# Kernel tuning notes

Hardware: AMD Instinct MI355X
Metric: run time of the kernel (lower is better)

The kernel has to match this reference:

```python
import jax, jax.numpy as jnp
import numpy as np

N_NODES = 32
GAT_OUT = 64
LSTM_H = 128
N_CLS = 4
NEG_SLOPE = 0.2


def setup_inputs() -> dict:
    key = jax.random.key(0)
    ks = jax.random.split(key, 12)
    B, T, E = 32, 512, 96
    F, H = GAT_OUT, LSTM_H
    s = 0.05
    return {
        "x_seq": jax.random.normal(ks[0], (B, T, N_NODES), jnp.float32),
        "edge_index": jax.random.randint(ks[1], (2, E), 0, N_NODES, jnp.int32),
        # GATConv params (heads=1): lin weight [in=1, F], attention vectors [F], bias [F]
        "w_gat": jax.random.normal(ks[2], (1, F), jnp.float32) * s,
        "att_src": jax.random.normal(ks[3], (F,), jnp.float32) * s,
        "att_dst": jax.random.normal(ks[4], (F,), jnp.float32) * s,
        "b_gat": jnp.zeros((F,), jnp.float32),
        # LSTM params, torch gate order (i, f, g, o)
        "W_ih": jax.random.normal(ks[5], (N_NODES * F, 4 * H), jnp.float32) * s,
        "W_hh": jax.random.normal(ks[6], (H, 4 * H), jnp.float32) * s,
        "b_ih": jnp.zeros((4 * H,), jnp.float32),
        "b_hh": jnp.zeros((4 * H,), jnp.float32),
        # classifier
        "W_fc": jax.random.normal(ks[7], (H, N_CLS), jnp.float32) * s,
        "b_fc": jnp.zeros((N_CLS,), jnp.float32),
    }


def _forward(x_seq, edge_index, w_gat, att_src, att_dst, b_gat,
             W_ih, W_hh, b_ih, b_hh, W_fc, b_fc):
    B, T, N = x_seq.shape
    F = w_gat.shape[1]
    H = W_hh.shape[0]

    # --- GAT over all (B,T) steps at once (PyG GATConv, heads=1, self-loops) ---
    loops = jnp.arange(N, dtype=edge_index.dtype)
    src = jnp.concatenate([edge_index[0], loops])  # [Et]
    dst = jnp.concatenate([edge_index[1], loops])  # [Et]
    Et = src.shape[0]

    h = x_seq[..., None] * w_gat            # [B,T,N,F] (in_channels=1 linear)
    a_s = h @ att_src                        # [B,T,N]
    a_d = h @ att_dst                        # [B,T,N]
    e = a_s[..., src] + a_d[..., dst]        # [B,T,Et]
    e = jnp.where(e > 0, e, NEG_SLOPE * e)   # LeakyReLU(0.2)

    # segment softmax over destination node, batched over B*T
    e2 = jnp.moveaxis(e, -1, 0).reshape(Et, B * T)
    m = jax.ops.segment_max(e2, dst, num_segments=N)        # [N,B*T]
    ex = jnp.exp(e2 - m[dst])
    z = jax.ops.segment_sum(ex, dst, num_segments=N)        # [N,B*T]
    alpha = ex / z[dst]                                      # [Et,B*T]
    alpha = jnp.moveaxis(alpha.reshape(Et, B, T), 0, -1)     # [B,T,Et]

    msg = alpha[..., None] * h[:, :, src, :]                 # [B,T,Et,F]
    onehot = (dst[:, None] == jnp.arange(N)).astype(h.dtype)  # [Et,N]
    out = jnp.einsum('btef,en->btnf', msg, onehot) + b_gat    # [B,T,N,F]

    seq = out.reshape(B, T, N * F)           # [B,T,2048]

    # --- single-layer LSTM (batch_first), torch gate order i,f,g,o ---
    xw = seq @ W_ih + (b_ih + b_hh)          # [B,T,4H]

    def step(carry, xw_t):
        hs, cs = carry
        g = xw_t + hs @ W_hh                 # [B,4H]
        i, f, gg, o = jnp.split(g, 4, axis=-1)
        cs = jax.nn.sigmoid(f) * cs + jax.nn.sigmoid(i) * jnp.tanh(gg)
        hs = jax.nn.sigmoid(o) * jnp.tanh(cs)
        return (hs, cs), None

    h0 = jnp.zeros((B, H), seq.dtype)
    (h_last, _), _ = jax.lax.scan(step, (h0, h0), jnp.moveaxis(xw, 1, 0))

    return h_last @ W_fc + b_fc              # [B,num_classes]


def reference(x_seq, edge_index, w_gat, att_src, att_dst, b_gat,
              W_ih, W_hh, b_ih, b_hh, W_fc, b_fc):
    return _forward(x_seq, edge_index, w_gat, att_src, att_dst, b_gat,
                    W_ih, W_hh, b_ih, b_hh, W_fc, b_fc)
```

## Files before the change

### kernel.cpp

```cpp
#include <hip/hip_runtime.h>

#define NN 32
#define FF 64
#define HH 128
#define G4 512
#define BB 32
#define TT 512
#define ET 128
#define NPOS (BB*TT)

__device__ __forceinline__ float frcp(float x) { return __builtin_amdgcn_rcpf(x); }

__global__ __launch_bounds__(512) void prep_kernel(const float* __restrict__ w_gat,
                                                   const float* __restrict__ b_gat,
                                                   const float* __restrict__ W_ih,
                                                   float* __restrict__ W_eff,
                                                   float* __restrict__ biasp) {
  int j = threadIdx.x;
  int n = blockIdx.x;
  float accw = 0.f, accb = 0.f;
#pragma unroll 8
  for (int f = 0; f < FF; ++f) {
    float wv = W_ih[(n * FF + f) * G4 + j];
    accw = fmaf(w_gat[f], wv, accw);
    accb = fmaf(b_gat[f], wv, accb);
  }
  W_eff[n * G4 + j] = accw;
  biasp[n * G4 + j] = accb;
}

__global__ __launch_bounds__(512) void prep2_kernel(const float* __restrict__ biasp,
                                                    const float* __restrict__ b_ih,
                                                    const float* __restrict__ b_hh,
                                                    const float* __restrict__ w_gat,
                                                    const float* __restrict__ att_src,
                                                    const float* __restrict__ att_dst,
                                                    const int* __restrict__ ei,
                                                    float* __restrict__ bias_eff,
                                                    float* __restrict__ scal,
                                                    int* __restrict__ srt_g,
                                                    int* __restrict__ off_g) {
  __shared__ int cnt[NN];
  __shared__ int off[NN + 1];
  __shared__ int srt[ET];
  int j = threadIdx.x;
  if (j < NN) cnt[j] = 0;
  float acc = b_ih[j] + b_hh[j];
#pragma unroll
  for (int n = 0; n < NN; ++n) acc += biasp[n * G4 + j];
  bias_eff[j] = acc;
  if (j == 0) {
    float cs = 0.f, cd = 0.f;
    for (int f = 0; f < FF; ++f) {
      cs = fmaf(w_gat[f], att_src[f], cs);
      cd = fmaf(w_gat[f], att_dst[f], cd);
    }
    scal[0] = cs;
    scal[1] = cd;
  }
  __syncthreads();
  int s = 0, d = 0, tk = 0;
  if (j < ET) {
    if (j < 96) { s = ei[j]; d = ei[96 + j]; }
    else { s = j - 96; d = j - 96; }
    tk = atomicAdd(&cnt[d], 1);
  }
  __syncthreads();
  if (j == 0) {
    off[0] = 0;
    for (int n = 0; n < NN; ++n) off[n + 1] = off[n] + cnt[n];
  }
  __syncthreads();
  if (j < ET) srt[off[d] + tk] = s;
  __syncthreads();
  if (j < ET) srt_g[j] = srt[j];
  if (j < NN + 1) off_g[j] = off[j];
}

__global__ __launch_bounds__(128) void prep3_kernel(const float* __restrict__ W_hh,
                                                    float* __restrict__ Wt) {
  int tid = blockIdx.x;
  int m = threadIdx.x;
  int r = tid >> 2, kq = tid & 3;
  int g = m >> 5, kk = m & 31;
  Wt[tid * 128 + m] = W_hh[(kq * 32 + kk) * G4 + g * 128 + r];
}

__global__ __launch_bounds__(256) void gatxw_kernel(const float* __restrict__ x_seq,
                                                    const int* __restrict__ srt_g,
                                                    const int* __restrict__ off_g,
                                                    const float* __restrict__ scal,
                                                    const float* __restrict__ W_eff,
                                                    const float* __restrict__ bias_eff,
                                                    float* __restrict__ xw) {
  __shared__ int srt[ET];
  __shared__ int offs[NN + 1];
  __shared__ float xs[8 * 32];
  __shared__ float sl[8 * 32];
  int tid = threadIdx.x;
  int posbase = blockIdx.x * 8;
  float we0[NN], we1[NN];
#pragma unroll
  for (int nn = 0; nn < NN; ++nn) {
    we0[nn] = W_eff[nn * G4 + tid];
    we1[nn] = W_eff[nn * G4 + 256 + tid];
  }
  float b0 = bias_eff[tid], b1 = bias_eff[256 + tid];
  if (tid < ET) srt[tid] = srt_g[tid];
  if (tid < NN + 1) offs[tid] = off_g[tid];
  int p = tid >> 5, n = tid & 31;
  xs[tid] = x_seq[posbase * NN + tid];
  __syncthreads();
  float cs = scal[0], cd = scal[1];
  int base = p * 32;
  int e0 = offs[n], e1 = offs[n + 1];
  float xn = xs[base + n];
  float cdxn = cd * xn;
  float m = -3.0e38f;
  for (int e = e0; e < e1; ++e) {
    float ev = fmaf(cs, xs[base + srt[e]], cdxn);
    ev = ev > 0.f ? ev : 0.2f * ev;
    m = fmaxf(m, ev);
  }
  float z = 0.f, sa = 0.f;
  for (int e = e0; e < e1; ++e) {
    float xsv = xs[base + srt[e]];
    float ev = fmaf(cs, xsv, cdxn);
    ev = ev > 0.f ? ev : 0.2f * ev;
    float ex = __expf(ev - m);
    z += ex;
    sa = fmaf(ex, xsv, sa);
  }
  sl[p * 32 + n] = sa * frcp(z);
  __syncthreads();
  for (int pp = 0; pp < 8; ++pp) {
    const float4* sp = (const float4*)&sl[pp * 32];
    float a0 = b0, a1 = b1;
#pragma unroll
    for (int q = 0; q < 8; ++q) {
      float4 sv = sp[q];
      a0 = fmaf(sv.x, we0[4 * q], a0);
      a0 = fmaf(sv.y, we0[4 * q + 1], a0);
      a0 = fmaf(sv.z, we0[4 * q + 2], a0);
      a0 = fmaf(sv.w, we0[4 * q + 3], a0);
      a1 = fmaf(sv.x, we1[4 * q], a1);
      a1 = fmaf(sv.y, we1[4 * q + 1], a1);
      a1 = fmaf(sv.z, we1[4 * q + 2], a1);
      a1 = fmaf(sv.w, we1[4 * q + 3], a1);
    }
    size_t row = (size_t)(posbase + pp) * G4;
    xw[row + tid] = a0;
    xw[row + 256 + tid] = a1;
  }
}


#define PK16F(HP, W0, W1, W2, W3) \
  "v_pk_fma_f32 v[216:217], v[" HP "], v[" W0 "], 0\n\t" \
  "v_pk_fma_f32 v[218:219], v[" HP "], v[" W1 "], 0\n\t" \
  "v_pk_fma_f32 v[220:221], v[" HP "], v[" W2 "], 0\n\t" \
  "v_pk_fma_f32 v[222:223], v[" HP "], v[" W3 "], 0\n\t"

#define PK16A(HP, W0, W1, W2, W3) \
  "v_pk_fma_f32 v[216:217], v[" HP "], v[" W0 "], v[216:217]\n\t" \
  "v_pk_fma_f32 v[218:219], v[" HP "], v[" W1 "], v[218:219]\n\t" \
  "v_pk_fma_f32 v[220:221], v[" HP "], v[" W2 "], v[220:221]\n\t" \
  "v_pk_fma_f32 v[222:223], v[" HP "], v[" W3 "], v[222:223]\n\t"

#define PHASE(XSLOT, RD, WR) \
  "ds_read_b128 v[32:35], " RD "\n\t" \
  "ds_read_b128 v[36:39], " RD " offset:16\n\t" \
  "ds_read_b128 v[40:43], " RD " offset:32\n\t" \
  "ds_read_b128 v[44:47], " RD " offset:48\n\t" \
  "ds_read_b128 v[48:51], " RD " offset:64\n\t" \
  "ds_read_b128 v[52:55], " RD " offset:80\n\t" \
  "ds_read_b128 v[56:59], " RD " offset:96\n\t" \
  "ds_read_b128 v[60:63], " RD " offset:112\n\t" \
  "s_waitcnt vmcnt(3)\n\t" \
  "v_mov_b32 v215, " XSLOT "\n\t" \
  "global_load_dword " XSLOT ", v194, %[xwb]\n\t" \
  "v_add_u32 v194, 0x800, v194\n\t" \
  "s_waitcnt lgkmcnt(7)\n\t" \
  PK16F("32:33", "64:65",  "96:97",   "128:129", "160:161") \
  PK16A("34:35", "66:67",  "98:99",   "130:131", "162:163") \
  "s_waitcnt lgkmcnt(6)\n\t" \
  PK16A("36:37", "68:69",  "100:101", "132:133", "164:165") \
  PK16A("38:39", "70:71",  "102:103", "134:135", "166:167") \
  "s_waitcnt lgkmcnt(5)\n\t" \
  PK16A("40:41", "72:73",  "104:105", "136:137", "168:169") \
  PK16A("42:43", "74:75",  "106:107", "138:139", "170:171") \
  "s_waitcnt lgkmcnt(4)\n\t" \
  PK16A("44:45", "76:77",  "108:109", "140:141", "172:173") \
  PK16A("46:47", "78:79",  "110:111", "142:143", "174:175") \
  "s_waitcnt lgkmcnt(3)\n\t" \
  PK16A("48:49", "80:81",  "112:113", "144:145", "176:177") \
  PK16A("50:51", "82:83",  "114:115", "146:147", "178:179") \
  "s_waitcnt lgkmcnt(2)\n\t" \
  PK16A("52:53", "84:85",  "116:117", "148:149", "180:181") \
  PK16A("54:55", "86:87",  "118:119", "150:151", "182:183") \
  "s_waitcnt lgkmcnt(1)\n\t" \
  PK16A("56:57", "88:89",  "120:121", "152:153", "184:185") \
  PK16A("58:59", "90:91",  "122:123", "154:155", "186:187") \
  "s_waitcnt lgkmcnt(0)\n\t" \
  PK16A("60:61", "92:93",  "124:125", "156:157", "188:189") \
  PK16A("62:63", "94:95",  "126:127", "158:159", "190:191") \
  "v_add_f32 v204, v216, v217\n\t" \
  "v_add_f32 v205, v218, v219\n\t" \
  "v_add_f32 v206, v220, v221\n\t" \
  "v_add_f32 v207, v222, v223\n\t" \
  "v_fmac_f32 v204, v215, v200\n\t" \
  "v_fmac_f32 v205, v215, v201\n\t" \
  "v_fmac_f32 v206, v215, v202\n\t" \
  "v_fmac_f32 v207, v215, v203\n\t" \
  "v_add_f32_dpp v204, v204, v204 quad_perm:[1,0,3,2] row_mask:0xf bank_mask:0xf\n\t" \
  "v_add_f32_dpp v205, v205, v205 quad_perm:[1,0,3,2] row_mask:0xf bank_mask:0xf\n\t" \
  "v_add_f32_dpp v206, v206, v206 quad_perm:[1,0,3,2] row_mask:0xf bank_mask:0xf\n\t" \
  "v_add_f32_dpp v207, v207, v207 quad_perm:[1,0,3,2] row_mask:0xf bank_mask:0xf\n\t" \
  "v_add_f32_dpp v204, v204, v204 quad_perm:[2,3,0,1] row_mask:0xf bank_mask:0xf\n\t" \
  "v_add_f32_dpp v205, v205, v205 quad_perm:[2,3,0,1] row_mask:0xf bank_mask:0xf\n\t" \
  "v_add_f32_dpp v206, v206, v206 quad_perm:[2,3,0,1] row_mask:0xf bank_mask:0xf\n\t" \
  "v_add_f32_dpp v207, v207, v207 quad_perm:[2,3,0,1] row_mask:0xf bank_mask:0xf\n\t" \
  "v_mul_f32 v208, 0xbfb8aa3b, v204\n\t" \
  "v_mul_f32 v209, 0xbfb8aa3b, v205\n\t" \
  "v_mul_f32 v210, 0x4038aa3b, v206\n\t" \
  "v_mul_f32 v211, 0xbfb8aa3b, v207\n\t" \
  "v_exp_f32 v208, v208\n\t" \
  "v_exp_f32 v209, v209\n\t" \
  "v_exp_f32 v210, v210\n\t" \
  "v_exp_f32 v211, v211\n\t" \
  "v_add_f32 v208, 1.0, v208\n\t" \
  "v_add_f32 v209, 1.0, v209\n\t" \
  "v_add_f32 v210, 1.0, v210\n\t" \
  "v_add_f32 v211, 1.0, v211\n\t" \
  "v_rcp_f32 v208, v208\n\t" \
  "v_rcp_f32 v209, v209\n\t" \
  "v_rcp_f32 v210, v210\n\t" \
  "v_rcp_f32 v211, v211\n\t" \
  "v_fma_f32 v210, -2.0, v210, 1.0\n\t" \
  "v_mul_f32 v212, v208, v210\n\t" \
  "v_fma_f32 v199, v209, v199, v212\n\t" \
  "v_mul_f32 v214, 0x4038aa3b, v199\n\t" \
  "v_exp_f32 v214, v214\n\t" \
  "s_nop 1\n\t" \
  "v_add_f32 v214, 1.0, v214\n\t" \
  "v_rcp_f32 v214, v214\n\t" \
  "s_nop 1\n\t" \
  "v_fma_f32 v214, -2.0, v214, 1.0\n\t" \
  "v_mul_f32 v213, v211, v214\n\t" \
  "ds_write_b32 " WR ", v213\n\t" \
  "s_waitcnt lgkmcnt(0)\n\t" \
  "s_barrier\n\t"

__global__ __launch_bounds__(512, 2) void lstm_kernel(const float* __restrict__ xw,
                                                      const float* __restrict__ Wt,
                                                      const float* __restrict__ W_fc,
                                                      const float* __restrict__ b_fc,
                                                      float* __restrict__ out) {
  __shared__ __align__(16) float lds[320];
  int b = blockIdx.x, tid = threadIdx.x;
  int r = tid >> 2, kq = tid & 3;
  if (tid < 320) lds[tid] = 0.f;
  const float* xwb = xw + (size_t)b * TT * G4;
  unsigned xoff0 = (unsigned)((kq * 128 + r) * 4);
  unsigned wtoff = (unsigned)(tid * 512);
  unsigned lbase = (unsigned)(uintptr_t)&lds[0];
  unsigned rda = lbase + kq * 160;
  unsigned rdb = rda + 640;
  unsigned wra = lbase + (((r >> 5) * 40 + (r & 31)) << 2);
  unsigned wrb = wra + 640;
  float mh0 = (kq == 0) ? 1.f : 0.f;
  float mh1 = (kq == 1) ? 1.f : 0.f;
  float mh2 = (kq == 2) ? 1.f : 0.f;
  float mh3 = (kq == 3) ? 1.f : 0.f;
  __syncthreads();
  asm volatile(
    "v_mov_b32 v194, %[xo]\n\t"
    "v_mov_b32 v195, %[rda]\n\t"
    "v_mov_b32 v196, %[rdb]\n\t"
    "v_mov_b32 v197, %[wra]\n\t"
    "v_mov_b32 v198, %[wrb]\n\t"
    "v_mov_b32 v199, 0\n\t"
    "v_mov_b32 v200, %[m0]\n\t"
    "v_mov_b32 v201, %[m1]\n\t"
    "v_mov_b32 v202, %[m2]\n\t"
    "v_mov_b32 v203, %[m3]\n\t"
    "global_load_dword v224, v194, %[xwb]\n\t"
    "v_add_u32 v194, 0x800, v194\n\t"
    "global_load_dword v225, v194, %[xwb]\n\t"
    "v_add_u32 v194, 0x800, v194\n\t"
    "global_load_dword v226, v194, %[xwb]\n\t"
    "v_add_u32 v194, 0x800, v194\n\t"
    "global_load_dword v227, v194, %[xwb]\n\t"
    "v_add_u32 v194, 0x800, v194\n\t"
    "global_load_dwordx4 v[64:67], %[wto], %[wtb] offset:0\n\t"
    "global_load_dwordx4 v[68:71], %[wto], %[wtb] offset:16\n\t"
    "global_load_dwordx4 v[72:75], %[wto], %[wtb] offset:32\n\t"
    "global_load_dwordx4 v[76:79], %[wto], %[wtb] offset:48\n\t"
    "global_load_dwordx4 v[80:83], %[wto], %[wtb] offset:64\n\t"
    "global_load_dwordx4 v[84:87], %[wto], %[wtb] offset:80\n\t"
    "global_load_dwordx4 v[88:91], %[wto], %[wtb] offset:96\n\t"
    "global_load_dwordx4 v[92:95], %[wto], %[wtb] offset:112\n\t"
    "global_load_dwordx4 v[96:99], %[wto], %[wtb] offset:128\n\t"
    "global_load_dwordx4 v[100:103], %[wto], %[wtb] offset:144\n\t"
    "global_load_dwordx4 v[104:107], %[wto], %[wtb] offset:160\n\t"
    "global_load_dwordx4 v[108:111], %[wto], %[wtb] offset:176\n\t"
    "global_load_dwordx4 v[112:115], %[wto], %[wtb] offset:192\n\t"
    "global_load_dwordx4 v[116:119], %[wto], %[wtb] offset:208\n\t"
    "global_load_dwordx4 v[120:123], %[wto], %[wtb] offset:224\n\t"
    "global_load_dwordx4 v[124:127], %[wto], %[wtb] offset:240\n\t"
    "global_load_dwordx4 v[128:131], %[wto], %[wtb] offset:256\n\t"
    "global_load_dwordx4 v[132:135], %[wto], %[wtb] offset:272\n\t"
    "global_load_dwordx4 v[136:139], %[wto], %[wtb] offset:288\n\t"
    "global_load_dwordx4 v[140:143], %[wto], %[wtb] offset:304\n\t"
    "global_load_dwordx4 v[144:147], %[wto], %[wtb] offset:320\n\t"
    "global_load_dwordx4 v[148:151], %[wto], %[wtb] offset:336\n\t"
    "global_load_dwordx4 v[152:155], %[wto], %[wtb] offset:352\n\t"
    "global_load_dwordx4 v[156:159], %[wto], %[wtb] offset:368\n\t"
    "global_load_dwordx4 v[160:163], %[wto], %[wtb] offset:384\n\t"
    "global_load_dwordx4 v[164:167], %[wto], %[wtb] offset:400\n\t"
    "global_load_dwordx4 v[168:171], %[wto], %[wtb] offset:416\n\t"
    "global_load_dwordx4 v[172:175], %[wto], %[wtb] offset:432\n\t"
    "global_load_dwordx4 v[176:179], %[wto], %[wtb] offset:448\n\t"
    "global_load_dwordx4 v[180:183], %[wto], %[wtb] offset:464\n\t"
    "global_load_dwordx4 v[184:187], %[wto], %[wtb] offset:480\n\t"
    "global_load_dwordx4 v[188:191], %[wto], %[wtb] offset:496\n\t"
    "s_waitcnt vmcnt(4)\n\t"
    "s_movk_i32 s20, 0x80\n\t"
    "L_lstm_%=:\n\t"
    PHASE("v224", "v195", "v198")
    PHASE("v225", "v196", "v197")
    PHASE("v226", "v195", "v198")
    PHASE("v227", "v196", "v197")
    "s_sub_u32 s20, s20, 1\n\t"
    "s_cmp_lg_u32 s20, 0\n\t"
    "s_cbranch_scc1 L_lstm_%=\n\t"
    "s_waitcnt vmcnt(0) lgkmcnt(0)\n\t"
    :
    : [xwb]"s"(xwb), [wtb]"s"(Wt), [wto]"v"(wtoff), [xo]"v"(xoff0),
      [rda]"v"(rda), [rdb]"v"(rdb), [wra]"v"(wra), [wrb]"v"(wrb),
      [m0]"v"(mh0), [m1]"v"(mh1), [m2]"v"(mh2), [m3]"v"(mh3)
    : "memory", "scc", "s20",
      "v32","v33","v34","v35","v36","v37","v38","v39",
      "v40","v41","v42","v43","v44","v45","v46","v47",
      "v48","v49","v50","v51","v52","v53","v54","v55",
      "v56","v57","v58","v59","v60","v61","v62","v63",
      "v64","v65","v66","v67","v68","v69","v70","v71",
      "v72","v73","v74","v75","v76","v77","v78","v79",
      "v80","v81","v82","v83","v84","v85","v86","v87",
      "v88","v89","v90","v91","v92","v93","v94","v95",
      "v96","v97","v98","v99","v100","v101","v102","v103",
      "v104","v105","v106","v107","v108","v109","v110","v111",
      "v112","v113","v114","v115","v116","v117","v118","v119",
      "v120","v121","v122","v123","v124","v125","v126","v127",
      "v128","v129","v130","v131","v132","v133","v134","v135",
      "v136","v137","v138","v139","v140","v141","v142","v143",
      "v144","v145","v146","v147","v148","v149","v150","v151",
      "v152","v153","v154","v155","v156","v157","v158","v159",
      "v160","v161","v162","v163","v164","v165","v166","v167",
      "v168","v169","v170","v171","v172","v173","v174","v175",
      "v176","v177","v178","v179","v180","v181","v182","v183",
      "v184","v185","v186","v187","v188","v189","v190","v191",
      "v192","v193","v194","v195","v196","v197","v198","v199",
      "v200","v201","v202","v203","v204","v205","v206","v207",
      "v208","v209","v210","v211","v212","v213","v214","v215",
      "v216","v217","v218","v219","v220","v221","v222","v223",
      "v224","v225","v226","v227");
  __syncthreads();
  if (tid < 4) {
    float acc = b_fc[tid];
#pragma unroll 8
    for (int k = 0; k < HH; ++k)
      acc = fmaf(lds[(k >> 5) * 40 + (k & 31)], W_fc[k * 4 + tid], acc);
    out[b * 4 + tid] = acc;
  }
}

extern "C" void kernel_launch(void* const* d_in, const int* in_sizes, int n_in,
                              void* d_out, int out_size, void* d_ws, size_t ws_size,
                              hipStream_t stream) {
  const float* x_seq   = (const float*)d_in[0];
  const int*   ei      = (const int*)d_in[1];
  const float* w_gat   = (const float*)d_in[2];
  const float* att_src = (const float*)d_in[3];
  const float* att_dst = (const float*)d_in[4];
  const float* b_gat   = (const float*)d_in[5];
  const float* W_ih    = (const float*)d_in[6];
  const float* W_hh    = (const float*)d_in[7];
  const float* b_ih    = (const float*)d_in[8];
  const float* b_hh    = (const float*)d_in[9];
  const float* W_fc    = (const float*)d_in[10];
  const float* b_fc    = (const float*)d_in[11];

  float* ws = (float*)d_ws;
  float* Wt       = ws;
  float* xw       = Wt + 65536;
  float* W_eff    = xw + (size_t)(NPOS + 8) * G4;
  float* bias_eff = W_eff + NN * G4;
  float* scal     = bias_eff + G4;
  float* biasp    = scal + 2;
  int*   srt_g    = (int*)(biasp + NN * G4);
  int*   off_g    = srt_g + ET;

  prep_kernel<<<NN, G4, 0, stream>>>(w_gat, b_gat, W_ih, W_eff, biasp);
  prep2_kernel<<<1, G4, 0, stream>>>(biasp, b_ih, b_hh, w_gat, att_src, att_dst, ei,
                                     bias_eff, scal, srt_g, off_g);
  prep3_kernel<<<G4, 128, 0, stream>>>(W_hh, Wt);
  gatxw_kernel<<<NPOS / 8, 256, 0, stream>>>(x_seq, srt_g, off_g, scal, W_eff, bias_eff, xw);
  lstm_kernel<<<BB, G4, 0, stream>>>(xw, Wt, W_fc, b_fc, (float*)d_out);
}
```

Before: 396.1 us.

## Merge prep kernels into neighbours and vectorize LSTM gate activation per quad lane

Folds the W_hh transpose into prep_kernel, and moves the bias reduction, edge CSR build and attention scalars into every gatxw block, so two launches disappear. Each gatxw block now redoes that small setup work. In the LSTM step, each lane of a quad selects its own gate pre-activation, adds xw, and computes one sigmoid or tanh, using one exp and one rcp instead of four. DPP broadcasts then share the gate values across the quad. The xw prefetch is moved after the FMA block so its wait overlaps the LDS reads.

```diff
diff --git a/kernel.cpp b/kernel.cpp
--- a/kernel.cpp
+++ b/kernel.cpp
@@ -14,8 +14,10 @@
 __global__ __launch_bounds__(512) void prep_kernel(const float* __restrict__ w_gat,
                                                    const float* __restrict__ b_gat,
                                                    const float* __restrict__ W_ih,
+                                                   const float* __restrict__ W_hh,
                                                    float* __restrict__ W_eff,
-                                                   float* __restrict__ biasp) {
+                                                   float* __restrict__ biasp,
+                                                   float* __restrict__ Wt) {
   int j = threadIdx.x;
   int n = blockIdx.x;
   float accw = 0.f, accb = 0.f;
@@ -27,76 +29,33 @@
   }
   W_eff[n * G4 + j] = accw;
   biasp[n * G4 + j] = accb;
+  int g0 = (n * G4 + j) * 4;
+#pragma unroll
+  for (int q = 0; q < 4; ++q) {
+    int e = g0 + q;
+    int tl = e >> 7, idx = e & 127;
+    int r = tl >> 2, kq = tl & 3;
+    int g = idx >> 5, kk = idx & 31;
+    Wt[e] = W_hh[(kq * 32 + kk) * G4 + g * 128 + r];
+  }
 }
 
-__global__ __launch_bounds__(512) void prep2_kernel(const float* __restrict__ biasp,
-                                                    const float* __restrict__ b_ih,
-                                                    const float* __restrict__ b_hh,
+__global__ __launch_bounds__(256) void gatxw_kernel(const float* __restrict__ x_seq,
+                                                    const int* __restrict__ ei,
                                                     const float* __restrict__ w_gat,
                                                     const float* __restrict__ att_src,
                                                     const float* __restrict__ att_dst,
-                                                    const int* __restrict__ ei,
-                                                    float* __restrict__ bias_eff,
-                                                    float* __restrict__ scal,
-                                                    int* __restrict__ srt_g,
-                                                    int* __restrict__ off_g) {
-  __shared__ int cnt[NN];
-  __shared__ int off[NN + 1];
-  __shared__ int srt[ET];
-  int j = threadIdx.x;
-  if (j < NN) cnt[j] = 0;
-  float acc = b_ih[j] + b_hh[j];
-#pragma unroll
-  for (int n = 0; n < NN; ++n) acc += biasp[n * G4 + j];
-  bias_eff[j] = acc;
-  if (j == 0) {
-    float cs = 0.f, cd = 0.f;
-    for (int f = 0; f < FF; ++f) {
-      cs = fmaf(w_gat[f], att_src[f], cs);
-      cd = fmaf(w_gat[f], att_dst[f], cd);
-    }
-    scal[0] = cs;
-    scal[1] = cd;
-  }
-  __syncthreads();
-  int s = 0, d = 0, tk = 0;
-  if (j < ET) {
-    if (j < 96) { s = ei[j]; d = ei[96 + j]; }
-    else { s = j - 96; d = j - 96; }
-    tk = atomicAdd(&cnt[d], 1);
-  }
-  __syncthreads();
-  if (j == 0) {
-    off[0] = 0;
-    for (int n = 0; n < NN; ++n) off[n + 1] = off[n] + cnt[n];
-  }
-  __syncthreads();
-  if (j < ET) srt[off[d] + tk] = s;
-  __syncthreads();
-  if (j < ET) srt_g[j] = srt[j];
-  if (j < NN + 1) off_g[j] = off[j];
-}
-
-__global__ __launch_bounds__(128) void prep3_kernel(const float* __restrict__ W_hh,
-                                                    float* __restrict__ Wt) {
-  int tid = blockIdx.x;
-  int m = threadIdx.x;
-  int r = tid >> 2, kq = tid & 3;
-  int g = m >> 5, kk = m & 31;
-  Wt[tid * 128 + m] = W_hh[(kq * 32 + kk) * G4 + g * 128 + r];
-}
-
-__global__ __launch_bounds__(256) void gatxw_kernel(const float* __restrict__ x_seq,
-                                                    const int* __restrict__ srt_g,
-                                                    const int* __restrict__ off_g,
-                                                    const float* __restrict__ scal,
+                                                    const float* __restrict__ b_ih,
+                                                    const float* __restrict__ b_hh,
                                                     const float* __restrict__ W_eff,
-                                                    const float* __restrict__ bias_eff,
+                                                    const float* __restrict__ biasp,
                                                     float* __restrict__ xw) {
   __shared__ int srt[ET];
   __shared__ int offs[NN + 1];
-  __shared__ float xs[8 * 32];
-  __shared__ float sl[8 * 32];
+  __shared__ int cnt[NN];
+  __shared__ float xs[256];
+  __shared__ float sl[256];
+  __shared__ float scal_sh[2];
   int tid = threadIdx.x;
   int posbase = blockIdx.x * 8;
   float we0[NN], we1[NN];
@@ -105,13 +64,41 @@
     we0[nn] = W_eff[nn * G4 + tid];
     we1[nn] = W_eff[nn * G4 + 256 + tid];
   }
-  float b0 = bias_eff[tid], b1 = bias_eff[256 + tid];
-  if (tid < ET) srt[tid] = srt_g[tid];
-  if (tid < NN + 1) offs[tid] = off_g[tid];
+  float b0 = b_ih[tid] + b_hh[tid];
+  float b1 = b_ih[256 + tid] + b_hh[256 + tid];
+#pragma unroll 8
+  for (int n = 0; n < NN; ++n) {
+    b0 += biasp[n * G4 + tid];
+    b1 += biasp[n * G4 + 256 + tid];
+  }
+  if (tid < NN) cnt[tid] = 0;
+  __syncthreads();
+  int es = 0, ed = 0, tk = 0;
+  if (tid < ET) {
+    if (tid < 96) { es = ei[tid]; ed = ei[96 + tid]; }
+    else { es = tid - 96; ed = tid - 96; }
+    tk = atomicAdd(&cnt[ed], 1);
+  }
+  __syncthreads();
+  if (tid == 0) {
+    offs[0] = 0;
+    for (int n = 0; n < NN; ++n) offs[n + 1] = offs[n] + cnt[n];
+  }
+  if (tid == 1) {
+    float cs = 0.f, cd = 0.f;
+    for (int f = 0; f < FF; ++f) {
+      cs = fmaf(w_gat[f], att_src[f], cs);
+      cd = fmaf(w_gat[f], att_dst[f], cd);
+    }
+    scal_sh[0] = cs;
+    scal_sh[1] = cd;
+  }
+  __syncthreads();
+  if (tid < ET) srt[offs[ed] + tk] = es;
+  xs[tid] = x_seq[posbase * NN + tid];
+  __syncthreads();
+  float cs = scal_sh[0], cd = scal_sh[1];
   int p = tid >> 5, n = tid & 31;
-  xs[tid] = x_seq[posbase * NN + tid];
-  __syncthreads();
-  float cs = scal[0], cd = scal[1];
   int base = p * 32;
   int e0 = offs[n], e1 = offs[n + 1];
   float xn = xs[base + n];
@@ -176,10 +163,6 @@
   "ds_read_b128 v[52:55], " RD " offset:80\n\t" \
   "ds_read_b128 v[56:59], " RD " offset:96\n\t" \
   "ds_read_b128 v[60:63], " RD " offset:112\n\t" \
-  "s_waitcnt vmcnt(3)\n\t" \
-  "v_mov_b32 v215, " XSLOT "\n\t" \
-  "global_load_dword " XSLOT ", v194, %[xwb]\n\t" \
-  "v_add_u32 v194, 0x800, v194\n\t" \
   "s_waitcnt lgkmcnt(7)\n\t" \
   PK16F("32:33", "64:65",  "96:97",   "128:129", "160:161") \
   PK16A("34:35", "66:67",  "98:99",   "130:131", "162:163") \
@@ -204,14 +187,14 @@
   "s_waitcnt lgkmcnt(0)\n\t" \
   PK16A("60:61", "92:93",  "124:125", "156:157", "188:189") \
   PK16A("62:63", "94:95",  "126:127", "158:159", "190:191") \
+  "s_waitcnt vmcnt(3)\n\t" \
+  "v_mov_b32 v215, " XSLOT "\n\t" \
+  "global_load_dword " XSLOT ", v194, %[xwb]\n\t" \
+  "v_add_u32 v194, 0x800, v194\n\t" \
   "v_add_f32 v204, v216, v217\n\t" \
   "v_add_f32 v205, v218, v219\n\t" \
   "v_add_f32 v206, v220, v221\n\t" \
   "v_add_f32 v207, v222, v223\n\t" \
-  "v_fmac_f32 v204, v215, v200\n\t" \
-  "v_fmac_f32 v205, v215, v201\n\t" \
-  "v_fmac_f32 v206, v215, v202\n\t" \
-  "v_fmac_f32 v207, v215, v203\n\t" \
   "v_add_f32_dpp v204, v204, v204 quad_perm:[1,0,3,2] row_mask:0xf bank_mask:0xf\n\t" \
   "v_add_f32_dpp v205, v205, v205 quad_perm:[1,0,3,2] row_mask:0xf bank_mask:0xf\n\t" \
   "v_add_f32_dpp v206, v206, v206 quad_perm:[1,0,3,2] row_mask:0xf bank_mask:0xf\n\t" \
@@ -220,34 +203,33 @@
   "v_add_f32_dpp v205, v205, v205 quad_perm:[2,3,0,1] row_mask:0xf bank_mask:0xf\n\t" \
   "v_add_f32_dpp v206, v206, v206 quad_perm:[2,3,0,1] row_mask:0xf bank_mask:0xf\n\t" \
   "v_add_f32_dpp v207, v207, v207 quad_perm:[2,3,0,1] row_mask:0xf bank_mask:0xf\n\t" \
-  "v_mul_f32 v208, 0xbfb8aa3b, v204\n\t" \
-  "v_mul_f32 v209, 0xbfb8aa3b, v205\n\t" \
-  "v_mul_f32 v210, 0x4038aa3b, v206\n\t" \
-  "v_mul_f32 v211, 0xbfb8aa3b, v207\n\t" \
-  "v_exp_f32 v208, v208\n\t" \
+  "v_cndmask_b32 v208, v204, v205, s[22:23]\n\t" \
+  "v_cndmask_b32 v209, v206, v207, s[22:23]\n\t" \
+  "v_cndmask_b32 v208, v208, v209, s[24:25]\n\t" \
+  "v_add_f32 v208, v208, v215\n\t" \
+  "v_mul_f32 v209, v200, v208\n\t" \
   "v_exp_f32 v209, v209\n\t" \
-  "v_exp_f32 v210, v210\n\t" \
-  "v_exp_f32 v211, v211\n\t" \
-  "v_add_f32 v208, 1.0, v208\n\t" \
+  "s_nop 0\n\t" \
   "v_add_f32 v209, 1.0, v209\n\t" \
-  "v_add_f32 v210, 1.0, v210\n\t" \
-  "v_add_f32 v211, 1.0, v211\n\t" \
-  "v_rcp_f32 v208, v208\n\t" \
   "v_rcp_f32 v209, v209\n\t" \
-  "v_rcp_f32 v210, v210\n\t" \
-  "v_rcp_f32 v211, v211\n\t" \
-  "v_fma_f32 v210, -2.0, v210, 1.0\n\t" \
-  "v_mul_f32 v212, v208, v210\n\t" \
-  "v_fma_f32 v199, v209, v199, v212\n\t" \
-  "v_mul_f32 v214, 0x4038aa3b, v199\n\t" \
-  "v_exp_f32 v214, v214\n\t" \
+  "s_nop 0\n\t" \
+  "v_fma_f32 v210, v201, v209, v202\n\t" \
   "s_nop 1\n\t" \
-  "v_add_f32 v214, 1.0, v214\n\t" \
-  "v_rcp_f32 v214, v214\n\t" \
-  "s_nop 1\n\t" \
-  "v_fma_f32 v214, -2.0, v214, 1.0\n\t" \
-  "v_mul_f32 v213, v211, v214\n\t" \
-  "ds_write_b32 " WR ", v213\n\t" \
+  "v_add_f32_dpp v211, v210, v203 quad_perm:[0,0,0,0] row_mask:0xf bank_mask:0xf\n\t" \
+  "v_add_f32_dpp v212, v210, v203 quad_perm:[1,1,1,1] row_mask:0xf bank_mask:0xf\n\t" \
+  "v_add_f32_dpp v213, v210, v203 quad_perm:[2,2,2,2] row_mask:0xf bank_mask:0xf\n\t" \
+  "v_add_f32_dpp v214, v210, v203 quad_perm:[3,3,3,3] row_mask:0xf bank_mask:0xf\n\t" \
+  "v_mul_f32 v211, v211, v213\n\t" \
+  "v_fma_f32 v199, v212, v199, v211\n\t" \
+  "v_mul_f32 v209, 0x4038aa3b, v199\n\t" \
+  "v_exp_f32 v209, v209\n\t" \
+  "s_nop 0\n\t" \
+  "v_add_f32 v209, 1.0, v209\n\t" \
+  "v_rcp_f32 v209, v209\n\t" \
+  "s_nop 0\n\t" \
+  "v_fma_f32 v209, -2.0, v209, 1.0\n\t" \
+  "v_mul_f32 v209, v214, v209\n\t" \
+  "ds_write_b32 " WR ", v209\n\t" \
   "s_waitcnt lgkmcnt(0)\n\t" \
   "s_barrier\n\t"
 
@@ -268,10 +250,11 @@
   unsigned rdb = rda + 640;
   unsigned wra = lbase + (((r >> 5) * 40 + (r & 31)) << 2);
   unsigned wrb = wra + 640;
-  float mh0 = (kq == 0) ? 1.f : 0.f;
-  float mh1 = (kq == 1) ? 1.f : 0.f;
-  float mh2 = (kq == 2) ? 1.f : 0.f;
-  float mh3 = (kq == 3) ? 1.f : 0.f;
+  float kmulf = (kq == 2) ? __uint_as_float(0x4038aa3bu)
+                          : __uint_as_float(0xbfb8aa3bu);
+  float Af = (kq == 2) ? -2.f : 1.f;
+  float Bf = (kq == 2) ? 1.f : 0.f;
+  unsigned kqodd = kq & 1, kqhi = kq >> 1;
   __syncthreads();
   asm volatile(
     "v_mov_b32 v194, %[xo]\n\t"
@@ -280,10 +263,12 @@
     "v_mov_b32 v197, %[wra]\n\t"
     "v_mov_b32 v198, %[wrb]\n\t"
     "v_mov_b32 v199, 0\n\t"
-    "v_mov_b32 v200, %[m0]\n\t"
-    "v_mov_b32 v201, %[m1]\n\t"
-    "v_mov_b32 v202, %[m2]\n\t"
-    "v_mov_b32 v203, %[m3]\n\t"
+    "v_mov_b32 v200, %[km]\n\t"
+    "v_mov_b32 v201, %[Aa]\n\t"
+    "v_mov_b32 v202, %[Bb]\n\t"
+    "v_mov_b32 v203, 0\n\t"
+    "v_cmp_eq_u32 s[22:23], 1, %[kodd]\n\t"
+    "v_cmp_eq_u32 s[24:25], 1, %[khi]\n\t"
     "global_load_dword v224, v194, %[xwb]\n\t"
     "v_add_u32 v194, 0x800, v194\n\t"
     "global_load_dword v225, v194, %[xwb]\n\t"
@@ -324,7 +309,7 @@
     "global_load_dwordx4 v[180:183], %[wto], %[wtb] offset:464\n\t"
     "global_load_dwordx4 v[184:187], %[wto], %[wtb] offset:480\n\t"
     "global_load_dwordx4 v[188:191], %[wto], %[wtb] offset:496\n\t"
-    "s_waitcnt vmcnt(4)\n\t"
+    "s_waitcnt vmcnt(0)\n\t"
     "s_movk_i32 s20, 0x80\n\t"
     "L_lstm_%=:\n\t"
     PHASE("v224", "v195", "v198")
@@ -338,8 +323,9 @@
     :
     : [xwb]"s"(xwb), [wtb]"s"(Wt), [wto]"v"(wtoff), [xo]"v"(xoff0),
       [rda]"v"(rda), [rdb]"v"(rdb), [wra]"v"(wra), [wrb]"v"(wrb),
-      [m0]"v"(mh0), [m1]"v"(mh1), [m2]"v"(mh2), [m3]"v"(mh3)
-    : "memory", "scc", "s20",
+      [km]"v"(kmulf), [Aa]"v"(Af), [Bb]"v"(Bf),
+      [kodd]"v"(kqodd), [khi]"v"(kqhi)
+    : "memory", "scc", "s20", "s22", "s23", "s24", "s25",
       "v32","v33","v34","v35","v36","v37","v38","v39",
       "v40","v41","v42","v43","v44","v45","v46","v47",
       "v48","v49","v50","v51","v52","v53","v54","v55",
@@ -392,19 +378,13 @@
   const float* b_fc    = (const float*)d_in[11];
 
   float* ws = (float*)d_ws;
-  float* Wt       = ws;
-  float* xw       = Wt + 65536;
-  float* W_eff    = xw + (size_t)(NPOS + 8) * G4;
-  float* bias_eff = W_eff + NN * G4;
-  float* scal     = bias_eff + G4;
-  float* biasp    = scal + 2;
-  int*   srt_g    = (int*)(biasp + NN * G4);
-  int*   off_g    = srt_g + ET;
-
-  prep_kernel<<<NN, G4, 0, stream>>>(w_gat, b_gat, W_ih, W_eff, biasp);
-  prep2_kernel<<<1, G4, 0, stream>>>(biasp, b_ih, b_hh, w_gat, att_src, att_dst, ei,
-                                     bias_eff, scal, srt_g, off_g);
-  prep3_kernel<<<G4, 128, 0, stream>>>(W_hh, Wt);
-  gatxw_kernel<<<NPOS / 8, 256, 0, stream>>>(x_seq, srt_g, off_g, scal, W_eff, bias_eff, xw);
+  float* Wt    = ws;
+  float* xw    = Wt + 65536;
+  float* W_eff = xw + (size_t)(NPOS + 8) * G4;
+  float* biasp = W_eff + NN * G4;
+
+  prep_kernel<<<NN, G4, 0, stream>>>(w_gat, b_gat, W_ih, W_hh, W_eff, biasp, Wt);
+  gatxw_kernel<<<NPOS / 8, 256, 0, stream>>>(x_seq, ei, w_gat, att_src, att_dst,
+                                             b_ih, b_hh, W_eff, biasp, xw);
   lstm_kernel<<<BB, G4, 0, stream>>>(xw, Wt, W_fc, b_fc, (float*)d_out);
 }
```

Measured after the change: 377.2 us. 4.8% less time.
